# Kernel tuning notes

Measured on AMD Instinct MI355X. Metric: run time of the kernel, lower is better.

The kernel has to match this reference:

```python
import jax, jax.numpy as jnp
import numpy as np

B, N, M = 8, 1024, 1024
APP_DIM = 256          # value output dim
FIRST_APP_DIM = 49     # 7x7 ROI grid
IN_DIM = APP_DIM * FIRST_APP_DIM  # 12544
APP_MDIM = 1024        # total Q/K projection dim
HEADS = 4
MD = APP_MDIM // HEADS  # per-head Q/K dim = self.app_mdim = 256 (also the score scale)
DV = APP_DIM // HEADS   # per-head value dim = 64
W_SCALE = 0.02


def setup_inputs() -> dict:
    key = jax.random.key(0)
    k1, k2, k3, k4, k5 = jax.random.split(key, 5)
    return {
        "first_app": jax.random.normal(k1, (B, N, IN_DIM), dtype=jnp.float32),
        "second_app": jax.random.normal(k2, (B, M, IN_DIM), dtype=jnp.float32),
        "Wk": jax.random.normal(k3, (IN_DIM, APP_MDIM), dtype=jnp.float32) * W_SCALE,
        "bk": jnp.zeros((APP_MDIM,), dtype=jnp.float32),
        "Wq": jax.random.normal(k4, (IN_DIM, APP_MDIM), dtype=jnp.float32) * W_SCALE,
        "bq": jnp.zeros((APP_MDIM,), dtype=jnp.float32),
        "Wv": jax.random.normal(k5, (IN_DIM, APP_DIM), dtype=jnp.float32) * W_SCALE,
        "bv": jnp.zeros((APP_DIM,), dtype=jnp.float32),
    }


def reference(first_app, second_app, Wk, bk, Wq, bq, Wv, bv):
    Bb, Nn, _ = first_app.shape
    Mm = second_app.shape[1]
    # projections: [B,N,H,MD], [B,M,H,MD], [B,N,H,DV]
    K = (first_app @ Wk + bk).reshape(Bb, Nn, HEADS, MD)
    Q = (second_app @ Wq + bq).reshape(Bb, Mm, HEADS, MD)
    V = (first_app @ Wv + bv).reshape(Bb, Nn, HEADS, DV)
    # L2-normalize queries per head (norm is detached in the original)
    q_norm = jax.lax.stop_gradient(jnp.linalg.norm(Q, axis=-1, keepdims=True))
    Q = Q / q_norm
    # scores: faithful to sum(Q*K)/self.app_mdim, expressed as a contraction
    A = jnp.einsum('bmhd,bnhd->bhmn', Q, K) / MD  # [B,H,M,N]
    # exp / sum over N == softmax over N
    w = jax.nn.softmax(A, axis=-1)
    out = jnp.einsum('bhmn,bnhv->bmhv', w, V).reshape(Bb, Mm, APP_DIM)
    return out
```

## Files before the change

kernel.cpp:

```cpp
#include <hip/hip_runtime.h>
#include <stdint.h>


typedef __bf16 bf16;
typedef __bf16 bf16x4 __attribute__((ext_vector_type(4)));
typedef __bf16 bf16x8 __attribute__((ext_vector_type(8)));
typedef float  f32x4  __attribute__((ext_vector_type(4)));

__device__ __forceinline__ void async_ld16(const void* g, void* lds) {
  __builtin_amdgcn_global_load_lds(
      (__attribute__((address_space(1))) void*)(g),
      (__attribute__((address_space(3))) void*)(lds), 16, 0, 0);
}

__global__ __launch_bounds__(256) void cast_bf16_kernel(
    const float4* __restrict__ in, bf16x4* __restrict__ out, int n4) {
  int i0 = blockIdx.x * blockDim.x + threadIdx.x;
  int stride = gridDim.x * blockDim.x;
  for (int i = i0; i < n4; i += stride) {
    float4 v = in[i];
    bf16x4 o;
    o[0] = (bf16)v.x; o[1] = (bf16)v.y; o[2] = (bf16)v.z; o[3] = (bf16)v.w;
    out[i] = o;
  }
}

__global__ __launch_bounds__(256) void transpose_cast_kernel(
    const float* __restrict__ W, bf16* __restrict__ WT, int N) {
  __shared__ __align__(16) bf16 tile[64 * 76];
  const int k0 = blockIdx.x * 64;
  const int n0 = blockIdx.y * 64;
  const int t = threadIdx.x;
  const int tr = t >> 4, tc = t & 15;
#pragma unroll
  for (int rnd = 0; rnd < 4; ++rnd) {
    int r = rnd * 16 + tr;
    float4 v = *(const float4*)(W + (size_t)(k0 + r) * N + n0 + tc * 4);
    bf16x4 o;
    o[0] = (bf16)v.x; o[1] = (bf16)v.y; o[2] = (bf16)v.z; o[3] = (bf16)v.w;
    *(bf16x4*)&tile[r * 76 + tc * 4] = o;
  }
  __syncthreads();
#pragma unroll
  for (int rnd = 0; rnd < 4; ++rnd) {
    int rr = rnd * 16 + tr;
    int c0 = tc * 4;
    bf16x4 o;
    o[0] = tile[(c0 + 0) * 76 + rr];
    o[1] = tile[(c0 + 1) * 76 + rr];
    o[2] = tile[(c0 + 2) * 76 + rr];
    o[3] = tile[(c0 + 3) * 76 + rr];
    *(bf16x4*)(WT + (size_t)(n0 + rr) * 12544 + k0 + c0) = o;
  }
}

__global__ __launch_bounds__(256) void gemm_bt_kernel(
    const bf16* __restrict__ A, const bf16* __restrict__ Bt,
    const float* __restrict__ bias, bf16* __restrict__ C, int N) {
  __shared__ __align__(16) bf16 As[128 * 64];
  __shared__ __align__(16) bf16 Bs[128 * 64];
  const int tid = threadIdx.x;
  const int w = tid >> 6, l = tid & 63;
  const int wr = w >> 1, wc = w & 1;
  const int quad = l >> 4, lo = l & 15;
  const size_t K = 12544;
  const size_t rowT = (size_t)blockIdx.x * 128;
  const size_t colT = (size_t)blockIdx.y * 128;
  const int srow = l >> 3;
  const int scb = (l & 7) ^ srow;
  const bf16* Ag = A + rowT * K + (size_t)scb * 8;
  const bf16* Bg = Bt + colT * K + (size_t)scb * 8;

  f32x4 acc[4][4];
#pragma unroll
  for (int mi = 0; mi < 4; ++mi)
#pragma unroll
    for (int ni = 0; ni < 4; ++ni)
#pragma unroll
      for (int r = 0; r < 4; ++r) acc[mi][ni][r] = 0.0f;

  for (int k0 = 0; k0 < 12544; k0 += 64) {
    __syncthreads();
#pragma unroll
    for (int i = 0; i < 4; ++i) {
      int row = i * 32 + w * 8 + srow;
      async_ld16(Ag + (size_t)row * K + k0, &As[(i * 256 + w * 64) * 8]);
    }
#pragma unroll
    for (int i = 0; i < 4; ++i) {
      int row = i * 32 + w * 8 + srow;
      async_ld16(Bg + (size_t)row * K + k0, &Bs[(i * 256 + w * 64) * 8]);
    }
    __syncthreads();
#pragma unroll
    for (int ks = 0; ks < 2; ++ks) {
      bf16x8 af[4], bfr[4];
#pragma unroll
      for (int mi = 0; mi < 4; ++mi) {
        int m = wr * 64 + mi * 16 + lo;
        int cb = (ks * 4 + quad) ^ (m & 7);
        af[mi] = *(const bf16x8*)&As[m * 64 + cb * 8];
      }
#pragma unroll
      for (int ni = 0; ni < 4; ++ni) {
        int n = wc * 64 + ni * 16 + lo;
        int cb = (ks * 4 + quad) ^ (n & 7);
        bfr[ni] = *(const bf16x8*)&Bs[n * 64 + cb * 8];
      }
#pragma unroll
      for (int mi = 0; mi < 4; ++mi)
#pragma unroll
        for (int ni = 0; ni < 4; ++ni)
          acc[mi][ni] = __builtin_amdgcn_mfma_f32_16x16x32_bf16(
              af[mi], bfr[ni], acc[mi][ni], 0, 0, 0);
    }
  }
#pragma unroll
  for (int ni = 0; ni < 4; ++ni) {
    int col = (int)colT + wc * 64 + ni * 16 + lo;
    float bb = bias[col];
#pragma unroll
    for (int mi = 0; mi < 4; ++mi) {
#pragma unroll
      for (int r = 0; r < 4; ++r) {
        size_t row = rowT + wr * 64 + mi * 16 + quad * 4 + r;
        C[row * (size_t)N + col] = (bf16)(acc[mi][ni][r] + bb);
      }
    }
  }
}

__global__ __launch_bounds__(256) void normq_kernel(bf16* __restrict__ Q) {
  const int w = threadIdx.x >> 6, l = threadIdx.x & 63;
  size_t base = ((size_t)blockIdx.x * 4 + w) * 256 + l * 4;
  bf16x4 v = *(bf16x4*)(Q + base);
  float f0 = (float)v[0], f1 = (float)v[1], f2 = (float)v[2], f3 = (float)v[3];
  float ss = f0 * f0 + f1 * f1 + f2 * f2 + f3 * f3;
#pragma unroll
  for (int m = 1; m < 64; m <<= 1) ss += __shfl_xor(ss, m, 64);
  float rn = rsqrtf(ss);
  bf16x4 o;
  o[0] = (bf16)(f0 * rn); o[1] = (bf16)(f1 * rn);
  o[2] = (bf16)(f2 * rn); o[3] = (bf16)(f3 * rn);
  *(bf16x4*)(Q + base) = o;
}

__global__ __launch_bounds__(256) void attn_kernel(
    const bf16* __restrict__ Qn, const bf16* __restrict__ Kb,
    const bf16* __restrict__ Vb, float* __restrict__ out) {
  __shared__ __align__(16) bf16 Qs[64 * 256];
  __shared__ __align__(16) bf16 Ks[32 * 256];
  __shared__ __align__(16) bf16 Vst[64 * 40];
  __shared__ __align__(16) bf16 Ps[4 * 16 * 40];
  const int tid = threadIdx.x;
  const int w = tid >> 6, l = tid & 63;
  const int quad = l >> 4, lo = l & 15;
  const int m0 = blockIdx.x * 64;
  const int h = blockIdx.y, b = blockIdx.z;
  const bf16* Qg = Qn + ((size_t)b * 1024 + m0) * 1024 + h * 256;
  const bf16* Kg = Kb + (size_t)b * 1024 * 1024 + h * 256;
  const bf16* Vg = Vb + (size_t)b * 1024 * 256 + h * 64;

  {
    int rbase = w * 2 + (l >> 5);
    int cbp = l & 31;
#pragma unroll
    for (int i = 0; i < 8; ++i) {
      int row = i * 8 + rbase;
      int cb = cbp ^ (row & 7);
      async_ld16(Qg + (size_t)row * 1024 + cb * 8, &Qs[(i * 256 + w * 64) * 8]);
    }
  }

  const int m = w * 16 + lo;
  bf16x8 af[8];
  f32x4 acc_o[4];
#pragma unroll
  for (int vi = 0; vi < 4; ++vi)
#pragma unroll
    for (int r = 0; r < 4; ++r) acc_o[vi][r] = 0.0f;
  float lsum[4] = {0.f, 0.f, 0.f, 0.f};

  for (int nt = 0; nt < 32; ++nt) {
    const int n0 = nt * 32;
    __syncthreads();
    {
      int rbase = w * 2 + (l >> 5);
      int cbp = l & 31;
#pragma unroll
      for (int i = 0; i < 4; ++i) {
        int row = i * 8 + rbase;
        int cb = cbp ^ (row & 7);
        async_ld16(Kg + (size_t)(n0 + row) * 1024 + cb * 8,
                   &Ks[(i * 256 + w * 64) * 8]);
      }
    }
    {
#pragma unroll
      for (int rnd = 0; rnd < 2; ++rnd) {
        int n = rnd * 16 + (tid >> 4);
        int v0 = (tid & 15) * 4;
        bf16x4 vv = *(const bf16x4*)(Vg + (size_t)(n0 + n) * 256 + v0);
#pragma unroll
        for (int j = 0; j < 4; ++j) Vst[(v0 + j) * 40 + n] = vv[j];
      }
    }
    __syncthreads();
    if (nt == 0) {
#pragma unroll
      for (int ks = 0; ks < 8; ++ks) {
        int cb = (ks * 4 + quad) ^ (m & 7);
        af[ks] = *(const bf16x8*)&Qs[m * 256 + cb * 8];
      }
    }
    f32x4 acc_s[2];
#pragma unroll
    for (int ni = 0; ni < 2; ++ni)
#pragma unroll
      for (int r = 0; r < 4; ++r) acc_s[ni][r] = 0.0f;
#pragma unroll
    for (int ks = 0; ks < 8; ++ks) {
#pragma unroll
      for (int ni = 0; ni < 2; ++ni) {
        int n = ni * 16 + lo;
        int cb = (ks * 4 + quad) ^ (n & 7);
        bf16x8 bfr = *(const bf16x8*)&Ks[n * 256 + cb * 8];
        acc_s[ni] =
            __builtin_amdgcn_mfma_f32_16x16x32_bf16(af[ks], bfr, acc_s[ni], 0, 0, 0);
      }
    }
#pragma unroll
    for (int ni = 0; ni < 2; ++ni) {
#pragma unroll
      for (int r = 0; r < 4; ++r) {
        float p = __expf(acc_s[ni][r] * (1.0f / 256.0f));
        lsum[r] += p;
        Ps[w * 640 + (quad * 4 + r) * 40 + ni * 16 + lo] = (bf16)p;
      }
    }
    __syncthreads();
    bf16x8 ap = *(const bf16x8*)&Ps[w * 640 + lo * 40 + quad * 8];
#pragma unroll
    for (int vi = 0; vi < 4; ++vi) {
      bf16x8 bv = *(const bf16x8*)&Vst[(vi * 16 + lo) * 40 + quad * 8];
      acc_o[vi] = __builtin_amdgcn_mfma_f32_16x16x32_bf16(ap, bv, acc_o[vi], 0, 0, 0);
    }
  }
#pragma unroll
  for (int r = 0; r < 4; ++r) {
#pragma unroll
    for (int mm = 1; mm < 16; mm <<= 1) lsum[r] += __shfl_xor(lsum[r], mm, 64);
  }
  float rl[4];
#pragma unroll
  for (int r = 0; r < 4; ++r) rl[r] = 1.0f / lsum[r];
#pragma unroll
  for (int vi = 0; vi < 4; ++vi) {
#pragma unroll
    for (int r = 0; r < 4; ++r) {
      size_t row = (size_t)b * 1024 + m0 + w * 16 + quad * 4 + r;
      out[row * 256 + h * 64 + vi * 16 + lo] = acc_o[vi][r] * rl[r];
    }
  }
}

extern "C" void kernel_launch(void* const* d_in, const int* in_sizes, int n_in,
                              void* d_out, int out_size, void* d_ws, size_t ws_size,
                              hipStream_t stream) {
  const float* first  = (const float*)d_in[0];
  const float* second = (const float*)d_in[1];
  const float* Wk = (const float*)d_in[2];
  const float* bk = (const float*)d_in[3];
  const float* Wq = (const float*)d_in[4];
  const float* bq = (const float*)d_in[5];
  const float* Wv = (const float*)d_in[6];
  const float* bv = (const float*)d_in[7];
  float* out = (float*)d_out;

  char* ws = (char*)d_ws;
  bf16* Afs  = (bf16*)(ws);
  bf16* Asnd = (bf16*)(ws + 205520896ULL);
  bf16* WkT  = (bf16*)(ws + 411041792ULL);
  bf16* WqT  = (bf16*)(ws + 436731904ULL);
  bf16* WvT  = (bf16*)(ws + 462422016ULL);
  bf16* Kw   = (bf16*)(ws + 468844544ULL);
  bf16* Qw   = (bf16*)(ws + 485621760ULL);
  bf16* Vw   = (bf16*)(ws + 502398976ULL);

  const int n4 = 102760448 / 4;
  cast_bf16_kernel<<<4096, 256, 0, stream>>>((const float4*)first, (bf16x4*)Afs, n4);
  cast_bf16_kernel<<<4096, 256, 0, stream>>>((const float4*)second, (bf16x4*)Asnd, n4);

  transpose_cast_kernel<<<dim3(196, 16), 256, 0, stream>>>(Wk, WkT, 1024);
  transpose_cast_kernel<<<dim3(196, 16), 256, 0, stream>>>(Wq, WqT, 1024);
  transpose_cast_kernel<<<dim3(196, 4), 256, 0, stream>>>(Wv, WvT, 256);

  gemm_bt_kernel<<<dim3(64, 8), 256, 0, stream>>>(Afs, WkT, bk, Kw, 1024);
  gemm_bt_kernel<<<dim3(64, 8), 256, 0, stream>>>(Asnd, WqT, bq, Qw, 1024);
  gemm_bt_kernel<<<dim3(64, 2), 256, 0, stream>>>(Afs, WvT, bv, Vw, 256);

  normq_kernel<<<8192, 256, 0, stream>>>(Qw);

  attn_kernel<<<dim3(16, 4, 8), 256, 0, stream>>>(Qw, Kw, Vw, out);
}
```

Before: 1.797 ms.

## Fuse K and Q projections into one 256x256-tile double-buffered GEMM kernel

```diff
diff --git a/kernel.cpp b/kernel.cpp
--- a/kernel.cpp
+++ b/kernel.cpp
@@ -51,6 +51,124 @@
     o[2] = tile[(c0 + 2) * 76 + rr];
     o[3] = tile[(c0 + 3) * 76 + rr];
     *(bf16x4*)(WT + (size_t)(n0 + rr) * 12544 + k0 + c0) = o;
+  }
+}
+
+__global__ __launch_bounds__(512, 2) void gemm_kq_kernel(
+    const bf16* __restrict__ Afs, const bf16* __restrict__ Asnd,
+    const bf16* __restrict__ WkT, const bf16* __restrict__ WqT,
+    const float* __restrict__ bk, const float* __restrict__ bq,
+    bf16* __restrict__ Kw, bf16* __restrict__ Qw) {
+  __shared__ __align__(16) bf16 As[2][256 * 64];
+  __shared__ __align__(16) bf16 Bs[2][256 * 64];
+  const int z = blockIdx.z;
+  const bf16* __restrict__ A    = z ? Asnd : Afs;
+  const bf16* __restrict__ Bt   = z ? WqT : WkT;
+  const float* __restrict__ bias = z ? bq : bk;
+  bf16* __restrict__ C = z ? Qw : Kw;
+
+  const size_t K = 12544;
+  const int tid = threadIdx.x;
+  const int w = tid >> 6, l = tid & 63;
+  const int wr = w >> 2, wc = w & 3;
+  const int quad = l >> 4, lo = l & 15;
+  const size_t rowT = (size_t)blockIdx.x * 256;
+  const size_t colT = (size_t)blockIdx.y * 256;
+
+  const int srow = tid >> 3;
+  const int scb = (tid & 7) ^ (srow & 7);
+  const bf16* Ag = A + (rowT + srow) * K + scb * 8;
+  const bf16* Bg = Bt + (colT + srow) * K + scb * 8;
+  const int ldsw = w * 8 * 64;
+
+#define STAGE_A(i, d_, kofs) \
+  async_ld16(Ag + (size_t)(i) * 64 * K + (kofs), &As[d_][(i) * 64 * 64 + ldsw])
+#define STAGE_B(i, d_, kofs) \
+  async_ld16(Bg + (size_t)(i) * 64 * K + (kofs), &Bs[d_][(i) * 64 * 64 + ldsw])
+
+  f32x4 acc[8][4];
+#pragma unroll
+  for (int mi = 0; mi < 8; ++mi)
+#pragma unroll
+    for (int ni = 0; ni < 4; ++ni)
+#pragma unroll
+      for (int r = 0; r < 4; ++r) acc[mi][ni][r] = 0.0f;
+
+#pragma unroll
+  for (int i = 0; i < 4; ++i) STAGE_A(i, 0, 0);
+#pragma unroll
+  for (int i = 0; i < 4; ++i) STAGE_B(i, 0, 0);
+  asm volatile("s_waitcnt vmcnt(0)" ::: "memory");
+  __builtin_amdgcn_s_barrier();
+
+  for (int kt = 0; kt < 196; ++kt) {
+    const int d = kt & 1;
+    const int knext = (kt + 1) * 64;
+    const bool pf = kt < 195;
+#pragma unroll
+    for (int q = 0; q < 4; ++q) {
+      const int mq = q >> 1, nq = q & 1;
+      bf16x8 af[4][2], bfr[2][2];
+#pragma unroll
+      for (int a = 0; a < 4; ++a) {
+        const int m = wr * 128 + (mq * 4 + a) * 16 + lo;
+#pragma unroll
+        for (int ks = 0; ks < 2; ++ks) {
+          const int g = ks * 4 + quad;
+          af[a][ks] = *(const bf16x8*)&As[d][m * 64 + (g ^ (m & 7)) * 8];
+        }
+      }
+#pragma unroll
+      for (int bi = 0; bi < 2; ++bi) {
+        const int n = wc * 64 + (nq * 2 + bi) * 16 + lo;
+#pragma unroll
+        for (int ks = 0; ks < 2; ++ks) {
+          const int g = ks * 4 + quad;
+          bfr[bi][ks] = *(const bf16x8*)&Bs[d][n * 64 + (g ^ (n & 7)) * 8];
+        }
+      }
+      if (q == 0 && pf) {
+        STAGE_A(0, d ^ 1, knext); STAGE_A(1, d ^ 1, knext);
+        STAGE_B(0, d ^ 1, knext); STAGE_B(1, d ^ 1, knext);
+      }
+      if (q == 1 && pf) {
+        STAGE_A(2, d ^ 1, knext); STAGE_A(3, d ^ 1, knext);
+        STAGE_B(2, d ^ 1, knext); STAGE_B(3, d ^ 1, knext);
+      }
+      __builtin_amdgcn_s_barrier();
+      __builtin_amdgcn_s_setprio(1);
+#pragma unroll
+      for (int ks = 0; ks < 2; ++ks)
+#pragma unroll
+        for (int a = 0; a < 4; ++a)
+#pragma unroll
+          for (int bi = 0; bi < 2; ++bi)
+            acc[mq * 4 + a][nq * 2 + bi] = __builtin_amdgcn_mfma_f32_16x16x32_bf16(
+                af[a][ks], bfr[bi][ks], acc[mq * 4 + a][nq * 2 + bi], 0, 0, 0);
+      __builtin_amdgcn_s_setprio(0);
+      if (q < 3) {
+        __builtin_amdgcn_s_barrier();
+      } else {
+        asm volatile("s_waitcnt vmcnt(0)" ::: "memory");
+        __builtin_amdgcn_s_barrier();
+      }
+    }
+  }
+#undef STAGE_A
+#undef STAGE_B
+
+#pragma unroll
+  for (int ni = 0; ni < 4; ++ni) {
+    const int col = (int)colT + wc * 64 + ni * 16 + lo;
+    const float bb = bias[col];
+#pragma unroll
+    for (int mi = 0; mi < 8; ++mi) {
+#pragma unroll
+      for (int r = 0; r < 4; ++r) {
+        const size_t row = rowT + wr * 128 + mi * 16 + quad * 4 + r;
+        C[row * 1024 + col] = (bf16)(acc[mi][ni][r] + bb);
+      }
+    }
   }
 }
 
@@ -295,8 +413,8 @@
   transpose_cast_kernel<<<dim3(196, 16), 256, 0, stream>>>(Wq, WqT, 1024);
   transpose_cast_kernel<<<dim3(196, 4), 256, 0, stream>>>(Wv, WvT, 256);
 
-  gemm_bt_kernel<<<dim3(64, 8), 256, 0, stream>>>(Afs, WkT, bk, Kw, 1024);
-  gemm_bt_kernel<<<dim3(64, 8), 256, 0, stream>>>(Asnd, WqT, bq, Qw, 1024);
+  gemm_kq_kernel<<<dim3(32, 4, 2), 512, 0, stream>>>(Afs, Asnd, WkT, WqT, bk, bq,
+                                                     Kw, Qw);
   gemm_bt_kernel<<<dim3(64, 2), 256, 0, stream>>>(Afs, WvT, bv, Vw, 256);
 
   normq_kernel<<<8192, 256, 0, stream>>>(Qw);
```

Result: faster. 1.735 ms (-3.5%).
